# Kernel tuning notes

Hardware: AMD Instinct MI355X
Metric: run time of the kernel (lower is better)

Reference implementation:

```python
import jax, jax.numpy as jnp
import numpy as np

SIZE = (2, 2)


def setup_inputs() -> dict:
    key = jax.random.key(0)
    k1, k2 = jax.random.split(key)
    B, H, W, C = 16, 64, 64, 128
    out_size = B * H * SIZE[0] * W * SIZE[1] * C  # 33_554_432
    updates = jax.random.normal(k1, (B, H, W, C), dtype=jnp.float32)
    mask = jax.random.randint(k2, (B, H, W, C), 0, out_size, dtype=jnp.int32)
    return {"updates": updates, "mask": mask}


def reference(updates, mask):
    # MaxUnpooling2D: scatter flattened updates into a zero buffer of the
    # full (upsampled) output size using flattened argmax indices, then reshape.
    B, H, W, C = updates.shape
    out_h, out_w = H * SIZE[0], W * SIZE[1]
    out_size = B * out_h * out_w * C
    # tf.scatter_nd sums duplicate indices -> use .add (matches semantics)
    flat = jnp.zeros((out_size,), dtype=updates.dtype).at[mask.reshape(-1)].add(
        updates.reshape(-1)
    )
    return flat.reshape(B, out_h, out_w, C)
```

## Files before the change

kernel.cpp:

```cpp
#include <hip/hip_runtime.h>
#include <hip/hip_fp16.h>


#define NB        2048
#define NB_SHIFT  14
#define RB        16384
#define P1B       1024
#define IPB       8192

__global__ __launch_bounds__(256, 4) void partition_kernel(
        const float4* __restrict__ upd4,
        const int4*   __restrict__ mask4,
        unsigned int* __restrict__ tableA,
        unsigned int* __restrict__ pairs) {
    __shared__ unsigned int hb[NB];
    __shared__ unsigned int wpart[4];
    __shared__ unsigned int stage[IPB];
    const int t = threadIdx.x;
    const int k = blockIdx.x;
    const int s4 = k * (IPB / 4);

    for (int b = t; b < NB; b += 256) hb[b] = 0u;
    __syncthreads();

    int4 mm[IPB / 4 / 256];
    #pragma unroll
    for (int j = 0; j < IPB / 4 / 256; ++j) mm[j] = mask4[s4 + j * 256 + t];
    #pragma unroll
    for (int j = 0; j < IPB / 4 / 256; ++j) {
        atomicAdd(&hb[((unsigned)mm[j].x) >> NB_SHIFT], 1u);
        atomicAdd(&hb[((unsigned)mm[j].y) >> NB_SHIFT], 1u);
        atomicAdd(&hb[((unsigned)mm[j].z) >> NB_SHIFT], 1u);
        atomicAdd(&hb[((unsigned)mm[j].w) >> NB_SHIFT], 1u);
    }
    __syncthreads();

    unsigned c[8], s = 0;
    #pragma unroll
    for (int j = 0; j < 8; ++j) { c[j] = hb[t * 8 + j]; s += c[j]; }
    unsigned inc = s;
    #pragma unroll
    for (int d = 1; d < 64; d <<= 1) {
        unsigned v = __shfl_up(inc, d, 64);
        if ((t & 63) >= d) inc += v;
    }
    if ((t & 63) == 63) wpart[t >> 6] = inc;
    __syncthreads();
    unsigned wbase = 0;
    #pragma unroll
    for (int w = 0; w < 4; ++w) if (w < (t >> 6)) wbase += wpart[w];
    unsigned run = wbase + inc - s;

    unsigned tw[8];
    #pragma unroll
    for (int j = 0; j < 8; ++j) {
        hb[t * 8 + j] = run;
        tw[j] = run | (c[j] << 16);
        run += c[j];
    }
    #pragma unroll
    for (int j = 0; j < 2; ++j)
        ((uint4*)(tableA + (size_t)k * NB))[t * 2 + j] =
            make_uint4(tw[j * 4 + 0], tw[j * 4 + 1], tw[j * 4 + 2], tw[j * 4 + 3]);
    __syncthreads();

    float4 uu[IPB / 4 / 256];
    #pragma unroll
    for (int j = 0; j < IPB / 4 / 256; ++j) uu[j] = upd4[s4 + j * 256 + t];
    #pragma unroll
    for (int j = 0; j < IPB / 4 / 256; ++j) {
        #define PLACE(mi, vi) { \
            unsigned b_ = ((unsigned)(mi)) >> NB_SHIFT; \
            unsigned pos_ = atomicAdd(&hb[b_], 1u); \
            stage[pos_] = (((unsigned)(mi)) & (RB - 1u)) | \
                          ((unsigned)__half_as_ushort(__float2half(vi)) << 16); }
        PLACE(mm[j].x, uu[j].x)
        PLACE(mm[j].y, uu[j].y)
        PLACE(mm[j].z, uu[j].z)
        PLACE(mm[j].w, uu[j].w)
        #undef PLACE
    }
    __syncthreads();

    const uint4* sp = (const uint4*)stage;
    uint4* dp = (uint4*)(pairs + (size_t)k * IPB);
    #pragma unroll
    for (int j = 0; j < IPB / 4 / 256; ++j) dp[j * 256 + t] = sp[j * 256 + t];
}

__global__ __launch_bounds__(256) void transpose_kernel(
        const unsigned int* __restrict__ A, unsigned int* __restrict__ B) {
    __shared__ unsigned int tile[32][33];
    const int tx = threadIdx.x & 31, ty = threadIdx.x >> 5;
    const int bx = blockIdx.x;
    const int by = blockIdx.y;
    #pragma unroll
    for (int r = 0; r < 32; r += 8)
        tile[ty + r][tx] = A[(size_t)(by * 32 + ty + r) * NB + bx * 32 + tx];
    __syncthreads();
    #pragma unroll
    for (int r = 0; r < 32; r += 8)
        B[(size_t)(bx * 32 + ty + r) * P1B + by * 32 + tx] = tile[tx][ty + r];
}

__global__ __launch_bounds__(256) void unbin_kernel(
        const unsigned int* __restrict__ tableB,
        const unsigned int* __restrict__ pairs,
        float4*             __restrict__ out4) {
    __shared__ float tile[RB];
    const int t = threadIdx.x;
    const int b = ((blockIdx.x & 7) << 8) | (blockIdx.x >> 3);
    float4* t4 = (float4*)tile;

    for (int j = t; j < RB / 4; j += 256) t4[j] = make_float4(0.f, 0.f, 0.f, 0.f);

    uint4 e = ((const uint4*)(tableB + (size_t)b * P1B))[t];
    unsigned s0 = (unsigned)(t * 4 + 0) * IPB + (e.x & 0xFFFFu), e0 = s0 + (e.x >> 16);
    unsigned s1 = (unsigned)(t * 4 + 1) * IPB + (e.y & 0xFFFFu), e1 = s1 + (e.y >> 16);
    unsigned s2 = (unsigned)(t * 4 + 2) * IPB + (e.z & 0xFFFFu), e2 = s2 + (e.z >> 16);
    unsigned s3 = (unsigned)(t * 4 + 3) * IPB + (e.w & 0xFFFFu), e3 = s3 + (e.w >> 16);
    unsigned a0 = s0 & ~3u, a1 = s1 & ~3u, a2 = s2 & ~3u, a3 = s3 & ~3u;
    __syncthreads();

    const uint4* p4 = (const uint4*)pairs;
    #define ADDP(w) atomicAdd(&tile[(w) & (RB - 1u)], \
                              __half2float(__ushort_as_half((unsigned short)((w) >> 16))))
    while ((a0 < e0) | (a1 < e1) | (a2 < e2) | (a3 < e3)) {
        bool c0 = a0 < e0, c1 = a1 < e1, c2 = a2 < e2, c3 = a3 < e3;
        uint4 v0, v1, v2, v3;
        if (c0) v0 = p4[a0 >> 2];
        if (c1) v1 = p4[a1 >> 2];
        if (c2) v2 = p4[a2 >> 2];
        if (c3) v3 = p4[a3 >> 2];
        if (c0) {
            if (a0 >= s0)                ADDP(v0.x);
            if (a0 + 1 >= s0 && a0 + 1 < e0) ADDP(v0.y);
            if (a0 + 2 >= s0 && a0 + 2 < e0) ADDP(v0.z);
            if (a0 + 3 < e0)             ADDP(v0.w);
            a0 += 4;
        }
        if (c1) {
            if (a1 >= s1)                ADDP(v1.x);
            if (a1 + 1 >= s1 && a1 + 1 < e1) ADDP(v1.y);
            if (a1 + 2 >= s1 && a1 + 2 < e1) ADDP(v1.z);
            if (a1 + 3 < e1)             ADDP(v1.w);
            a1 += 4;
        }
        if (c2) {
            if (a2 >= s2)                ADDP(v2.x);
            if (a2 + 1 >= s2 && a2 + 1 < e2) ADDP(v2.y);
            if (a2 + 2 >= s2 && a2 + 2 < e2) ADDP(v2.z);
            if (a2 + 3 < e2)             ADDP(v2.w);
            a2 += 4;
        }
        if (c3) {
            if (a3 >= s3)                ADDP(v3.x);
            if (a3 + 1 >= s3 && a3 + 1 < e3) ADDP(v3.y);
            if (a3 + 2 >= s3 && a3 + 2 < e3) ADDP(v3.z);
            if (a3 + 3 < e3)             ADDP(v3.w);
            a3 += 4;
        }
    }
    #undef ADDP
    __syncthreads();

    for (int j = t; j < RB / 4; j += 256)
        out4[(size_t)b * (RB / 4) + j] = t4[j];
}

__global__ void zero_out_kernel(float4* __restrict__ out, int n4) {
    int i = blockIdx.x * blockDim.x + threadIdx.x;
    if (i < n4) out[i] = make_float4(0.f, 0.f, 0.f, 0.f);
}
__global__ void scatter_add_kernel(const float4* __restrict__ upd,
                                   const int4* __restrict__ mask,
                                   float* __restrict__ out, int n4) {
    int i = blockIdx.x * blockDim.x + threadIdx.x;
    if (i < n4) {
        float4 u = upd[i];
        int4 m = mask[i];
        atomicAdd(out + m.x, u.x);
        atomicAdd(out + m.y, u.y);
        atomicAdd(out + m.z, u.z);
        atomicAdd(out + m.w, u.w);
    }
}

extern "C" void kernel_launch(void* const* d_in, const int* in_sizes, int n_in,
                              void* d_out, int out_size, void* d_ws, size_t ws_size,
                              hipStream_t stream) {
    const float* updates = (const float*)d_in[0];
    const int*   mask    = (const int*)d_in[1];
    float* out = (float*)d_out;
    const int n  = in_sizes[0];
    const int n4 = n >> 2;
    const int o4 = out_size >> 2;

    const size_t pairs_b  = (size_t)P1B * IPB * sizeof(unsigned);
    const size_t table_b  = (size_t)P1B * NB * sizeof(unsigned);
    const size_t need = pairs_b + 2 * table_b;
    if (ws_size >= need && out_size == NB * RB && n == P1B * IPB) {
        unsigned* pairs  = (unsigned*)d_ws;
        unsigned* tableA = (unsigned*)((char*)d_ws + pairs_b);
        unsigned* tableB = (unsigned*)((char*)d_ws + pairs_b + table_b);

        partition_kernel<<<P1B, 256, 0, stream>>>(
            (const float4*)updates, (const int4*)mask, tableA, pairs);
        transpose_kernel<<<dim3(NB / 32, P1B / 32), 256, 0, stream>>>(tableA, tableB);
        unbin_kernel<<<NB, 256, 0, stream>>>(tableB, pairs, (float4*)out);
    } else {
        zero_out_kernel<<<(o4 + 255) / 256, 256, 0, stream>>>((float4*)out, o4);
        scatter_add_kernel<<<(n4 + 255) / 256, 256, 0, stream>>>(
            (const float4*)updates, (const int4*)mask, out, n4);
    }
}
```

Measured before the change: 243.3 us.

## Drop transpose kernel by writing bin table in bucket-major uint4 layout

The partition kernel now writes its per-bin offset/count table directly in a transposed uint4 layout indexed by bin group and partition block, so the separate transpose kernel and its extra table buffer go away. The unbin kernel moves to 512 threads, each handling two partition segments and picking its lane from the uint4 by bin index modulo 4. Pairs and final output are written with nontemporal stores. This removes one launch and one table round-trip, but the partition kernel's table writes become strided scatter stores, and the unbin kernel reads four times more table data and discards three quarters of it.

```diff
diff --git a/kernel.cpp b/kernel.cpp
--- a/kernel.cpp
+++ b/kernel.cpp
@@ -8,10 +8,13 @@
 #define P1B       1024
 #define IPB       8192
 
+typedef float        __attribute__((ext_vector_type(4))) f32x4v;
+typedef unsigned int __attribute__((ext_vector_type(4))) u32x4v;
+
 __global__ __launch_bounds__(256, 4) void partition_kernel(
         const float4* __restrict__ upd4,
         const int4*   __restrict__ mask4,
-        unsigned int* __restrict__ tableA,
+        uint4*        __restrict__ tableT,
         unsigned int* __restrict__ pairs) {
     __shared__ unsigned int hb[NB];
     __shared__ unsigned int wpart[4];
@@ -58,10 +61,8 @@
         tw[j] = run | (c[j] << 16);
         run += c[j];
     }
-    #pragma unroll
-    for (int j = 0; j < 2; ++j)
-        ((uint4*)(tableA + (size_t)k * NB))[t * 2 + j] =
-            make_uint4(tw[j * 4 + 0], tw[j * 4 + 1], tw[j * 4 + 2], tw[j * 4 + 3]);
+    tableT[(size_t)(t * 2 + 0) * P1B + k] = make_uint4(tw[0], tw[1], tw[2], tw[3]);
+    tableT[(size_t)(t * 2 + 1) * P1B + k] = make_uint4(tw[4], tw[5], tw[6], tw[7]);
     __syncthreads();
 
     float4 uu[IPB / 4 / 256];
@@ -85,26 +86,14 @@
     const uint4* sp = (const uint4*)stage;
     uint4* dp = (uint4*)(pairs + (size_t)k * IPB);
     #pragma unroll
-    for (int j = 0; j < IPB / 4 / 256; ++j) dp[j * 256 + t] = sp[j * 256 + t];
+    for (int j = 0; j < IPB / 4 / 256; ++j) {
+        uint4 v = sp[j * 256 + t];
+        __builtin_nontemporal_store(*(const u32x4v*)&v, (u32x4v*)&dp[j * 256 + t]);
+    }
 }
 
-__global__ __launch_bounds__(256) void transpose_kernel(
-        const unsigned int* __restrict__ A, unsigned int* __restrict__ B) {
-    __shared__ unsigned int tile[32][33];
-    const int tx = threadIdx.x & 31, ty = threadIdx.x >> 5;
-    const int bx = blockIdx.x;
-    const int by = blockIdx.y;
-    #pragma unroll
-    for (int r = 0; r < 32; r += 8)
-        tile[ty + r][tx] = A[(size_t)(by * 32 + ty + r) * NB + bx * 32 + tx];
-    __syncthreads();
-    #pragma unroll
-    for (int r = 0; r < 32; r += 8)
-        B[(size_t)(bx * 32 + ty + r) * P1B + by * 32 + tx] = tile[tx][ty + r];
-}
-
-__global__ __launch_bounds__(256) void unbin_kernel(
-        const unsigned int* __restrict__ tableB,
+__global__ __launch_bounds__(512, 4) void unbin_kernel(
+        const uint4*        __restrict__ tableT,
         const unsigned int* __restrict__ pairs,
         float4*             __restrict__ out4) {
     __shared__ float tile[RB];
@@ -112,60 +101,50 @@
     const int b = ((blockIdx.x & 7) << 8) | (blockIdx.x >> 3);
     float4* t4 = (float4*)tile;
 
-    for (int j = t; j < RB / 4; j += 256) t4[j] = make_float4(0.f, 0.f, 0.f, 0.f);
+    const int sel = b & 3;
+    uint4 q0 = tableT[(size_t)(b >> 2) * P1B + 2 * t + 0];
+    uint4 q1 = tableT[(size_t)(b >> 2) * P1B + 2 * t + 1];
 
-    uint4 e = ((const uint4*)(tableB + (size_t)b * P1B))[t];
-    unsigned s0 = (unsigned)(t * 4 + 0) * IPB + (e.x & 0xFFFFu), e0 = s0 + (e.x >> 16);
-    unsigned s1 = (unsigned)(t * 4 + 1) * IPB + (e.y & 0xFFFFu), e1 = s1 + (e.y >> 16);
-    unsigned s2 = (unsigned)(t * 4 + 2) * IPB + (e.z & 0xFFFFu), e2 = s2 + (e.z >> 16);
-    unsigned s3 = (unsigned)(t * 4 + 3) * IPB + (e.w & 0xFFFFu), e3 = s3 + (e.w >> 16);
-    unsigned a0 = s0 & ~3u, a1 = s1 & ~3u, a2 = s2 & ~3u, a3 = s3 & ~3u;
+    for (int j = t; j < RB / 4; j += 512) t4[j] = make_float4(0.f, 0.f, 0.f, 0.f);
+
+    unsigned d0 = sel == 0 ? q0.x : sel == 1 ? q0.y : sel == 2 ? q0.z : q0.w;
+    unsigned d1 = sel == 0 ? q1.x : sel == 1 ? q1.y : sel == 2 ? q1.z : q1.w;
+    unsigned s0 = (unsigned)(t * 2 + 0) * IPB + (d0 & 0xFFFFu), e0 = s0 + (d0 >> 16);
+    unsigned s1 = (unsigned)(t * 2 + 1) * IPB + (d1 & 0xFFFFu), e1 = s1 + (d1 >> 16);
+    unsigned a0 = s0 & ~3u, a1 = s1 & ~3u;
     __syncthreads();
 
     const uint4* p4 = (const uint4*)pairs;
     #define ADDP(w) atomicAdd(&tile[(w) & (RB - 1u)], \
                               __half2float(__ushort_as_half((unsigned short)((w) >> 16))))
-    while ((a0 < e0) | (a1 < e1) | (a2 < e2) | (a3 < e3)) {
-        bool c0 = a0 < e0, c1 = a1 < e1, c2 = a2 < e2, c3 = a3 < e3;
-        uint4 v0, v1, v2, v3;
+    while ((a0 < e0) | (a1 < e1)) {
+        bool c0 = a0 < e0, c1 = a1 < e1;
+        uint4 v0, v1;
         if (c0) v0 = p4[a0 >> 2];
         if (c1) v1 = p4[a1 >> 2];
-        if (c2) v2 = p4[a2 >> 2];
-        if (c3) v3 = p4[a3 >> 2];
         if (c0) {
-            if (a0 >= s0)                ADDP(v0.x);
+            if (a0 >= s0)                    ADDP(v0.x);
             if (a0 + 1 >= s0 && a0 + 1 < e0) ADDP(v0.y);
             if (a0 + 2 >= s0 && a0 + 2 < e0) ADDP(v0.z);
-            if (a0 + 3 < e0)             ADDP(v0.w);
+            if (a0 + 3 < e0)                 ADDP(v0.w);
             a0 += 4;
         }
         if (c1) {
-            if (a1 >= s1)                ADDP(v1.x);
+            if (a1 >= s1)                    ADDP(v1.x);
             if (a1 + 1 >= s1 && a1 + 1 < e1) ADDP(v1.y);
             if (a1 + 2 >= s1 && a1 + 2 < e1) ADDP(v1.z);
-            if (a1 + 3 < e1)             ADDP(v1.w);
+            if (a1 + 3 < e1)                 ADDP(v1.w);
             a1 += 4;
-        }
-        if (c2) {
-            if (a2 >= s2)                ADDP(v2.x);
-            if (a2 + 1 >= s2 && a2 + 1 < e2) ADDP(v2.y);
-            if (a2 + 2 >= s2 && a2 + 2 < e2) ADDP(v2.z);
-            if (a2 + 3 < e2)             ADDP(v2.w);
-            a2 += 4;
-        }
-        if (c3) {
-            if (a3 >= s3)                ADDP(v3.x);
-            if (a3 + 1 >= s3 && a3 + 1 < e3) ADDP(v3.y);
-            if (a3 + 2 >= s3 && a3 + 2 < e3) ADDP(v3.z);
-            if (a3 + 3 < e3)             ADDP(v3.w);
-            a3 += 4;
         }
     }
     #undef ADDP
     __syncthreads();
 
-    for (int j = t; j < RB / 4; j += 256)
-        out4[(size_t)b * (RB / 4) + j] = t4[j];
+    for (int j = t; j < RB / 4; j += 512) {
+        float4 v = t4[j];
+        __builtin_nontemporal_store(*(const f32x4v*)&v,
+                                    (f32x4v*)&out4[(size_t)b * (RB / 4) + j]);
+    }
 }
 
 __global__ void zero_out_kernel(float4* __restrict__ out, int n4) {
@@ -196,18 +175,16 @@
     const int n4 = n >> 2;
     const int o4 = out_size >> 2;
 
-    const size_t pairs_b  = (size_t)P1B * IPB * sizeof(unsigned);
-    const size_t table_b  = (size_t)P1B * NB * sizeof(unsigned);
-    const size_t need = pairs_b + 2 * table_b;
+    const size_t pairs_b = (size_t)P1B * IPB * sizeof(unsigned);
+    const size_t table_b = (size_t)(NB / 4) * P1B * sizeof(uint4);
+    const size_t need = pairs_b + table_b;
     if (ws_size >= need && out_size == NB * RB && n == P1B * IPB) {
         unsigned* pairs  = (unsigned*)d_ws;
-        unsigned* tableA = (unsigned*)((char*)d_ws + pairs_b);
-        unsigned* tableB = (unsigned*)((char*)d_ws + pairs_b + table_b);
+        uint4*    tableT = (uint4*)((char*)d_ws + pairs_b);
 
         partition_kernel<<<P1B, 256, 0, stream>>>(
-            (const float4*)updates, (const int4*)mask, tableA, pairs);
-        transpose_kernel<<<dim3(NB / 32, P1B / 32), 256, 0, stream>>>(tableA, tableB);
-        unbin_kernel<<<NB, 256, 0, stream>>>(tableB, pairs, (float4*)out);
+            (const float4*)updates, (const int4*)mask, tableT, pairs);
+        unbin_kernel<<<NB, 512, 0, stream>>>(tableT, pairs, (float4*)out);
     } else {
         zero_out_kernel<<<(o4 + 255) / 256, 256, 0, stream>>>((float4*)out, o4);
         scatter_add_kernel<<<(n4 + 255) / 256, 256, 0, stream>>>(
```

Result: slower. 249.0 us (+2.4%).
